# Kernel tuning notes

Measured on AMD Instinct MI355X. Metric: run time of the kernel, lower is better.

## Reference

```python
import jax, jax.numpy as jnp
import numpy as np

B, T, D, H, DH, DMLP, L, V = 32, 80, 128, 8, 64, 512, 8, 50257


def _ln(x, g, b, eps=1e-5):
    m = jnp.mean(x, axis=-1, keepdims=True)
    v = jnp.var(x, axis=-1, keepdims=True)
    return (x - m) * jax.lax.rsqrt(v + eps) * g + b


def setup_inputs() -> dict:
    key = jax.random.key(0)
    ks = jax.random.split(key, 16)
    emb_std = 1.0 / np.sqrt(2 * D)
    sD = 1.0 / np.sqrt(D)
    return {
        "x": jax.random.randint(ks[0], (B, T), 0, V),
        "tok_emb": jax.random.normal(ks[1], (V, D), jnp.float32) * emb_std,
        "pos_emb": jax.random.normal(ks[2], (T, D), jnp.float32) * emb_std,
        # per-block, per-head Q/K/V projections (no bias), stacked over L blocks
        "Wq": jax.random.normal(ks[3], (L, H, D, DH), jnp.float32) * sD,
        "Wk": jax.random.normal(ks[4], (L, H, D, DH), jnp.float32) * sD,
        "Wv": jax.random.normal(ks[5], (L, H, D, DH), jnp.float32) * sD,
        "Wo": jax.random.normal(ks[6], (L, H * DH, D), jnp.float32) / np.sqrt(H * DH),
        "bo": jnp.zeros((L, D), jnp.float32),
        "ln1_g": jnp.ones((L, D), jnp.float32),
        "ln1_b": jnp.zeros((L, D), jnp.float32),
        "ln2_g": jnp.ones((L, D), jnp.float32),
        "ln2_b": jnp.zeros((L, D), jnp.float32),
        "W1": jax.random.normal(ks[7], (L, D, DMLP), jnp.float32) * sD,
        "b1": jnp.zeros((L, DMLP), jnp.float32),
        "W2": jax.random.normal(ks[8], (L, DMLP, D), jnp.float32) / np.sqrt(DMLP),
        "b2": jnp.zeros((L, D), jnp.float32),
        "lnf_g": jnp.ones((D,), jnp.float32),
        "lnf_b": jnp.zeros((D,), jnp.float32),
        "Wcls": jax.random.normal(ks[9], (D, V), jnp.float32) * sD,
        "bcls": jnp.zeros((V,), jnp.float32),
    }


def reference(x, tok_emb, pos_emb, Wq, Wk, Wv, Wo, bo, ln1_g, ln1_b,
              ln2_g, ln2_b, W1, b1, W2, b2, lnf_g, lnf_b, Wcls, bcls):
    h = tok_emb[x] + pos_emb[jnp.arange(T)]  # [B,T,D]
    scale = 1.0 / np.sqrt(DH)

    def block(h, p):
        wq, wk, wv, wo, bo_, g1, b1_, g2, b2_, w1, bm1, w2, bm2 = p
        a = _ln(h, g1, b1_)
        q = jnp.einsum('btd,hde->bhte', a, wq)
        k = jnp.einsum('btd,hde->bhte', a, wk)
        v = jnp.einsum('btd,hde->bhte', a, wv)
        scores = jnp.einsum('bhte,bhse->bhts', q, k) * scale  # [B,H,T,T]
        # faithful to masked_fill(tril(scores)==0, -inf)
        scores = jnp.where(jnp.tril(scores) == 0, -jnp.inf, scores)
        w = jax.nn.softmax(scores, axis=-1)  # dropout inactive (eval)
        o = jnp.einsum('bhts,bhse->bhte', w, v)
        o = o.transpose(0, 2, 1, 3).reshape(h.shape[0], T, H * DH)
        h = h + o @ wo + bo_
        m = _ln(h, g2, b2_)
        h = h + jax.nn.gelu(m @ w1 + bm1, approximate=False) @ w2 + bm2
        return h, None

    h, _ = jax.lax.scan(
        block, h,
        (Wq, Wk, Wv, Wo, bo, ln1_g, ln1_b, ln2_g, ln2_b, W1, b1, W2, b2))
    h = _ln(h, lnf_g, lnf_b)
    return h @ Wcls + bcls  # [B,T,V]
```

## Files before the change

kernel.cpp:

```cpp
#include <hip/hip_runtime.h>
#include <hip/hip_bf16.h>
#include <hip/hip_fp16.h>
#include <math.h>

constexpr int B = 32, T = 80, D = 128, H = 8, DH = 64, DMLP = 512, L = 8, V = 50257;
constexpr int M = B * T;
constexpr int HD = H * DH;
constexpr int QKVN = 3 * HD;
constexpr int VPAD = 50304;

typedef _Float16 f16x8 __attribute__((ext_vector_type(8)));
typedef float f32x4 __attribute__((ext_vector_type(4)));

__device__ __forceinline__ float gelu_f(float x) {
    return 0.5f * x * (1.0f + erff(x * 0.70710678118654752f));
}

__global__ __launch_bounds__(256)
void embed_ln(const int* __restrict__ x, const float* __restrict__ tok,
              const float* __restrict__ pos, const float* __restrict__ g,
              const float* __restrict__ bb, float* __restrict__ h,
              __half* __restrict__ out) {
    int wid = threadIdx.x >> 6, lane = threadIdx.x & 63;
    int row = blockIdx.x * 4 + wid;
    int t = row % T;
    const float* te = tok + (size_t)x[row] * D;
    const float* pe = pos + (size_t)t * D;
    float v0 = te[lane]      + pe[lane];
    float v1 = te[64 + lane] + pe[64 + lane];
    int i0 = row * D + lane, i1 = i0 + 64;
    h[i0] = v0; h[i1] = v1;
    float s = v0 + v1;
    #pragma unroll
    for (int off = 32; off; off >>= 1) s += __shfl_xor(s, off);
    float mean = s * (1.0f / 128.0f);
    float d0 = v0 - mean, d1 = v1 - mean;
    float q = d0 * d0 + d1 * d1;
    #pragma unroll
    for (int off = 32; off; off >>= 1) q += __shfl_xor(q, off);
    float inv = rsqrtf(q * (1.0f / 128.0f) + 1e-5f);
    out[i0] = __float2half(d0 * inv * g[lane]      + bb[lane]);
    out[i1] = __float2half(d1 * inv * g[64 + lane] + bb[64 + lane]);
}

__global__ __launch_bounds__(256)
void combine_ln(const float* __restrict__ p, const float* __restrict__ bias,
                const float* __restrict__ g, const float* __restrict__ bb,
                float* __restrict__ h, __half* __restrict__ out) {
    constexpr int plane = M * D;
    int wid = threadIdx.x >> 6, lane = threadIdx.x & 63;
    int row = blockIdx.x * 4 + wid;
    int i0 = row * D + lane, i1 = i0 + 64;
    float v0 = h[i0] + p[i0] + p[i0 + plane] + p[i0 + 2 * plane] + p[i0 + 3 * plane]
             + bias[lane];
    float v1 = h[i1] + p[i1] + p[i1 + plane] + p[i1 + 2 * plane] + p[i1 + 3 * plane]
             + bias[64 + lane];
    h[i0] = v0; h[i1] = v1;
    float s = v0 + v1;
    #pragma unroll
    for (int off = 32; off; off >>= 1) s += __shfl_xor(s, off);
    float mean = s * (1.0f / 128.0f);
    float d0 = v0 - mean, d1 = v1 - mean;
    float q = d0 * d0 + d1 * d1;
    #pragma unroll
    for (int off = 32; off; off >>= 1) q += __shfl_xor(q, off);
    float inv = rsqrtf(q * (1.0f / 128.0f) + 1e-5f);
    out[i0] = __float2half(d0 * inv * g[lane]      + bb[lane]);
    out[i1] = __float2half(d1 * inv * g[64 + lane] + bb[64 + lane]);
}

__global__ __launch_bounds__(256)
void prep_small(const float* __restrict__ Wq, const float* __restrict__ Wk,
                const float* __restrict__ Wv, const float* __restrict__ Wo,
                const float* __restrict__ W1, const float* __restrict__ W2,
                __half* __restrict__ WqkvT, __half* __restrict__ WoT,
                __half* __restrict__ W1T, __half* __restrict__ W2T) {
    int id = blockIdx.x * 256 + threadIdx.x;
    if (id < L * QKVN * D) {
        int d = id & 127; int lc = id >> 7; int c = lc % QKVN; int l = lc / QKVN;
        int e = c & 63, hh = (c >> 6) & 7, wsel = c >> 9;
        const float* src = (wsel == 0) ? Wq : (wsel == 1) ? Wk : Wv;
        WqkvT[id] = __float2half(src[(((size_t)l * H + hh) * D + d) * DH + e]);
    } else {
        int id2 = id - L * QKVN * D;
        int which = id2 >> 19;
        int r = id2 & 524287;
        if (which == 0) {
            int k = r & 511, n = (r >> 9) & 127, l = r >> 16;
            WoT[r] = __float2half(Wo[((size_t)l * 512 + k) * 128 + n]);
        } else if (which == 1) {
            int k = r & 127, n = (r >> 7) & 511, l = r >> 16;
            W1T[r] = __float2half(W1[((size_t)l * 128 + k) * 512 + n]);
        } else {
            int k = r & 511, n = (r >> 9) & 127, l = r >> 16;
            W2T[r] = __float2half(W2[((size_t)l * 512 + k) * 128 + n]);
        }
    }
}

__global__ __launch_bounds__(256)
void prep_wcls(const float* __restrict__ Wcls, __half* __restrict__ WT) {
    __shared__ float tile[128][33];
    int n0 = blockIdx.x * 32;
    for (int i = threadIdx.x; i < 128 * 32; i += 256) {
        int k = i >> 5, j = i & 31;
        int n = n0 + j;
        tile[k][j] = (n < V) ? Wcls[(size_t)k * V + n] : 0.0f;
    }
    __syncthreads();
    for (int i = threadIdx.x; i < 32 * 64; i += 256) {
        int j = i >> 6, kp = i & 63;
        __half2 hv = __floats2half2_rn(tile[2 * kp][j], tile[2 * kp + 1][j]);
        *reinterpret_cast<__half2*>(WT + (size_t)(n0 + j) * 128 + 2 * kp) = hv;
    }
}

template<int MT, int NT, int MODE>
__global__ __launch_bounds__(256)
void hgemm(const __half* __restrict__ A, int lda,
           const __half* __restrict__ BT, int ldb,
           const float* __restrict__ bias,
           float* __restrict__ outF, __half* __restrict__ outH, int ldc) {
    const int tid = threadIdx.x, l = tid & 63, wid = tid >> 6;
    const int wm = wid >> 1, wn = wid & 1;
    const int row0 = blockIdx.y * (2 * MT * 16) + wm * (MT * 16);
    const int col0 = blockIdx.x * (2 * NT * 16) + wn * (NT * 16);
    const int z = blockIdx.z;
    const int rl = l & 15, kl = (l >> 4) * 8;
    const __half* Ap = A + (size_t)(row0 + rl) * lda + z * 128 + kl;
    const __half* Bp = BT + (size_t)(col0 + rl) * ldb + z * 128 + kl;

    f32x4 acc[MT][NT];
    #pragma unroll
    for (int mi = 0; mi < MT; mi++)
        #pragma unroll
        for (int ni = 0; ni < NT; ni++) acc[mi][ni] = (f32x4){0.f, 0.f, 0.f, 0.f};

    #pragma unroll
    for (int ks = 0; ks < 4; ks++) {
        f16x8 af[MT], bf[NT];
        #pragma unroll
        for (int mi = 0; mi < MT; mi++)
            af[mi] = *reinterpret_cast<const f16x8*>(Ap + (size_t)mi * 16 * lda + ks * 32);
        #pragma unroll
        for (int ni = 0; ni < NT; ni++)
            bf[ni] = *reinterpret_cast<const f16x8*>(Bp + (size_t)ni * 16 * ldb + ks * 32);
        #pragma unroll
        for (int mi = 0; mi < MT; mi++)
            #pragma unroll
            for (int ni = 0; ni < NT; ni++)
                acc[mi][ni] = __builtin_amdgcn_mfma_f32_16x16x32_f16(
                    af[mi], bf[ni], acc[mi][ni], 0, 0, 0);
    }

    const int orow = (l >> 4) * 4;
    #pragma unroll
    for (int mi = 0; mi < MT; mi++) {
        #pragma unroll
        for (int ni = 0; ni < NT; ni++) {
            int col = col0 + ni * 16 + rl;
            #pragma unroll
            for (int i = 0; i < 4; i++) {
                int row = row0 + mi * 16 + orow + i;
                float v = acc[mi][ni][i];
                if (MODE == 1) {
                    outF[((size_t)z * M + row) * 128 + col] = v;
                } else if (MODE == 2) {
                    outH[(size_t)row * ldc + col] = __float2half(gelu_f(v + bias[col]));
                } else {
                    outH[(size_t)row * ldc + col] = __float2half(v);
                }
            }
        }
    }
}

__global__ __launch_bounds__(256)
void hgemm_cls(const __half* __restrict__ A, const __half* __restrict__ BT,
               const float* __restrict__ bias, float* __restrict__ out) {
    constexpr int MT = 4, NT = 4;
    constexpr int MB = M / 128;
    constexpr int NB = VPAD / 128;
    constexpr int NWG = MB * NB;
    constexpr int q = NWG / 8, r = NWG % 8;
    int orig = blockIdx.x;
    int xcd = orig & 7, off = orig >> 3;
    int wg = (xcd < r ? xcd * (q + 1) : r * (q + 1) + (xcd - r) * q) + off;
    int mb = wg % MB, nb = wg / MB;

    const int tid = threadIdx.x, l = tid & 63, wid = tid >> 6;
    const int wm = wid >> 1, wn = wid & 1;
    const int row0 = mb * 128 + wm * 64;
    const int col0 = nb * 128 + wn * 64;
    const int rl = l & 15, kl = (l >> 4) * 8;
    const __half* Ap = A + (size_t)(row0 + rl) * 128 + kl;
    const __half* Bp = BT + (size_t)(col0 + rl) * 128 + kl;

    f32x4 acc[MT][NT];
    #pragma unroll
    for (int mi = 0; mi < MT; mi++)
        #pragma unroll
        for (int ni = 0; ni < NT; ni++) acc[mi][ni] = (f32x4){0.f, 0.f, 0.f, 0.f};

    #pragma unroll
    for (int ks = 0; ks < 4; ks++) {
        f16x8 af[MT], bf[NT];
        #pragma unroll
        for (int mi = 0; mi < MT; mi++)
            af[mi] = *reinterpret_cast<const f16x8*>(Ap + (size_t)mi * 16 * 128 + ks * 32);
        #pragma unroll
        for (int ni = 0; ni < NT; ni++)
            bf[ni] = *reinterpret_cast<const f16x8*>(Bp + (size_t)ni * 16 * 128 + ks * 32);
        #pragma unroll
        for (int mi = 0; mi < MT; mi++)
            #pragma unroll
            for (int ni = 0; ni < NT; ni++)
                acc[mi][ni] = __builtin_amdgcn_mfma_f32_16x16x32_f16(
                    af[mi], bf[ni], acc[mi][ni], 0, 0, 0);
    }

    const int orow = (l >> 4) * 4;
    #pragma unroll
    for (int mi = 0; mi < MT; mi++) {
        #pragma unroll
        for (int ni = 0; ni < NT; ni++) {
            int col = col0 + ni * 16 + rl;
            if (col < V) {
                float bv = bias[col];
                #pragma unroll
                for (int i = 0; i < 4; i++) {
                    int row = row0 + mi * 16 + orow + i;
                    out[(size_t)row * V + col] = acc[mi][ni][i] + bv;
                }
            }
        }
    }
}

__device__ __forceinline__ void load_h8(const __half* p, float* dst) {
    float4 raw = *reinterpret_cast<const float4*>(p);
    const __half2* h2 = reinterpret_cast<const __half2*>(&raw);
    float2 f;
    f = __half22float2(h2[0]); dst[0] = f.x; dst[1] = f.y;
    f = __half22float2(h2[1]); dst[2] = f.x; dst[3] = f.y;
    f = __half22float2(h2[2]); dst[4] = f.x; dst[5] = f.y;
    f = __half22float2(h2[3]); dst[6] = f.x; dst[7] = f.y;
}

__global__ __launch_bounds__(256)
void attn_fused(const __half* __restrict__ qkv, __half* __restrict__ o) {
    __shared__ float qS[T][DH];
    __shared__ float pS[T][T];
    int bh = blockIdx.x;
    int b = bh >> 3, h = bh & 7;
    const __half* base  = qkv + (size_t)b * T * QKVN + h * DH;
    const __half* kbase = base + HD;
    const __half* vbase = base + 2 * HD;

    for (int i = threadIdx.x; i < T * 8; i += 256) {
        int t = i >> 3, c8 = i & 7;
        load_h8(base + (size_t)t * QKVN + c8 * 8, &qS[t][c8 * 8]);
    }
    __syncthreads();

    for (int i = threadIdx.x; i < T * T; i += 256) {
        int t = i / T, s = i - t * T;
        float val = -INFINITY;
        if (s <= t) {
            const __half* krow = kbase + (size_t)s * QKVN;
            float accv = 0.0f;
            #pragma unroll
            for (int e8 = 0; e8 < 8; e8++) {
                float kf[8]; load_h8(krow + e8 * 8, kf);
                const float* qf = &qS[t][e8 * 8];
                #pragma unroll
                for (int u = 0; u < 8; u++) accv = fmaf(kf[u], qf[u], accv);
            }
            val = accv * 0.125f;
        }
        pS[t][s] = val;
    }
    __syncthreads();

    for (int i = threadIdx.x; i < T * 8; i += 256) {
        int t = i >> 3, c8 = i & 7;
        load_h8(vbase + (size_t)t * QKVN + c8 * 8, &qS[t][c8 * 8]);
    }

    int wid = threadIdx.x >> 6, lane = threadIdx.x & 63;
    for (int t = wid; t < T; t += 4) {
        float v0 = pS[t][lane];
        float v1 = (lane < T - 64) ? pS[t][64 + lane] : -INFINITY;
        float mx = fmaxf(v0, v1);
        #pragma unroll
        for (int off = 32; off; off >>= 1) mx = fmaxf(mx, __shfl_xor(mx, off));
        float e0 = expf(v0 - mx);
        float e1 = (lane < T - 64) ? expf(v1 - mx) : 0.0f;
        float ss = e0 + e1;
        #pragma unroll
        for (int off = 32; off; off >>= 1) ss += __shfl_xor(ss, off);
        float rs = 1.0f / ss;
        pS[t][lane] = e0 * rs;
        if (lane < T - 64) pS[t][64 + lane] = e1 * rs;
    }
    __syncthreads();

    for (int i = threadIdx.x; i < T * DH; i += 256) {
        int t = i >> 6, e = i & 63;
        float accv = 0.0f;
        for (int s = 0; s <= t; s++) accv = fmaf(pS[t][s], qS[s][e], accv);
        o[((size_t)b * T + t) * HD + h * DH + e] = __float2half(accv);
    }
}

extern "C" void kernel_launch(void* const* d_in, const int* in_sizes, int n_in,
                              void* d_out, int out_size, void* d_ws, size_t ws_size,
                              hipStream_t stream) {
    const int*   x     = (const int*)d_in[0];
    const float* tok   = (const float*)d_in[1];
    const float* pos   = (const float*)d_in[2];
    const float* Wq    = (const float*)d_in[3];
    const float* Wk    = (const float*)d_in[4];
    const float* Wv    = (const float*)d_in[5];
    const float* Wo    = (const float*)d_in[6];
    const float* bo    = (const float*)d_in[7];
    const float* ln1g  = (const float*)d_in[8];
    const float* ln1b  = (const float*)d_in[9];
    const float* ln2g  = (const float*)d_in[10];
    const float* ln2b  = (const float*)d_in[11];
    const float* W1    = (const float*)d_in[12];
    const float* b1    = (const float*)d_in[13];
    const float* W2    = (const float*)d_in[14];
    const float* b2    = (const float*)d_in[15];
    const float* lnfg  = (const float*)d_in[16];
    const float* lnfb  = (const float*)d_in[17];
    const float* Wcls  = (const float*)d_in[18];
    const float* bcls  = (const float*)d_in[19];
    float* out = (float*)d_out;

    char* w = (char*)d_ws;
    float*  h     = (float*)w;                 w += (size_t)M * D * 4;
    __half* a_h   = (__half*)w;                w += (size_t)M * D * 2;
    __half* qkvh  = (__half*)w;                w += (size_t)M * QKVN * 2;
    __half* o_h   = (__half*)w;                w += (size_t)M * HD * 2;
    __half* mlp   = (__half*)w;                w += (size_t)M * DMLP * 2;
    float*  pbuf  = (float*)w;                 w += (size_t)4 * M * D * 4;
    __half* WqkvT = (__half*)w;                w += (size_t)L * QKVN * D * 2;
    __half* WoT   = (__half*)w;                w += (size_t)L * D * HD * 2;
    __half* W1T   = (__half*)w;                w += (size_t)L * DMLP * D * 2;
    __half* W2T   = (__half*)w;                w += (size_t)L * D * DMLP * 2;
    __half* WclsT = (__half*)w;                w += (size_t)VPAD * D * 2;

    prep_small<<<(L * QKVN * D + 3 * L * DMLP * D) / 256, 256, 0, stream>>>(
        Wq, Wk, Wv, Wo, W1, W2, WqkvT, WoT, W1T, W2T);
    prep_wcls<<<VPAD / 32, 256, 0, stream>>>(Wcls, WclsT);
    embed_ln<<<M / 4, 256, 0, stream>>>(x, tok, pos, ln1g, ln1b, h, a_h);

    for (int l = 0; l < L; l++) {
        hgemm<2, 2, 3><<<dim3(QKVN / 64, M / 64, 1), 256, 0, stream>>>(
            a_h, D, WqkvT + (size_t)l * QKVN * D, D, nullptr, nullptr, qkvh, QKVN);
        attn_fused<<<B * H, 256, 0, stream>>>(qkvh, o_h);
        hgemm<2, 2, 1><<<dim3(D / 64, M / 64, 4), 256, 0, stream>>>(
            o_h, HD, WoT + (size_t)l * D * HD, HD, nullptr, pbuf, nullptr, D);
        combine_ln<<<M / 4, 256, 0, stream>>>(
            pbuf, bo + l * D, ln2g + l * D, ln2b + l * D, h, a_h);

        hgemm<2, 2, 2><<<dim3(DMLP / 64, M / 64, 1), 256, 0, stream>>>(
            a_h, D, W1T + (size_t)l * DMLP * D, D, b1 + l * DMLP, nullptr, mlp, DMLP);
        hgemm<2, 2, 1><<<dim3(D / 64, M / 64, 4), 256, 0, stream>>>(
            mlp, DMLP, W2T + (size_t)l * D * DMLP, DMLP, nullptr, pbuf, nullptr, D);
        const float* ng = (l + 1 < L) ? ln1g + (l + 1) * D : lnfg;
        const float* nb = (l + 1 < L) ? ln1b + (l + 1) * D : lnfb;
        combine_ln<<<M / 4, 256, 0, stream>>>(pbuf, b2 + l * D, ng, nb, h, a_h);
    }

    hgemm_cls<<<(M / 128) * (VPAD / 128), 256, 0, stream>>>(a_h, WclsT, bcls, out);
}
```

Before: 1.427 ms.

## Fuse QKV projection into MFMA-based attention and deepen split-K for projections

Removes the separate QKV GEMM and its global intermediate. Each attention block now computes its head's Q, K and V directly from the normalized activations with MFMA, keeping them in LDS. The QK^T and PV products move from scalar fp32 loops to f16 MFMA tiles: probabilities are stored as f16 and V is kept transposed with zero padding. The Wo and W2 GEMMs switch from 4 to 8 split-K partitions for more parallelism, so the combine kernel must read twice as many partial planes. The trade-off is a lower-precision P·V path and recomputed weight loads in every attention block.

```diff
diff --git a/kernel.cpp b/kernel.cpp
--- a/kernel.cpp
+++ b/kernel.cpp
@@ -51,10 +51,10 @@
     int wid = threadIdx.x >> 6, lane = threadIdx.x & 63;
     int row = blockIdx.x * 4 + wid;
     int i0 = row * D + lane, i1 = i0 + 64;
-    float v0 = h[i0] + p[i0] + p[i0 + plane] + p[i0 + 2 * plane] + p[i0 + 3 * plane]
-             + bias[lane];
-    float v1 = h[i1] + p[i1] + p[i1 + plane] + p[i1 + 2 * plane] + p[i1 + 3 * plane]
-             + bias[64 + lane];
+    float v0 = h[i0] + bias[lane];
+    float v1 = h[i1] + bias[64 + lane];
+    #pragma unroll
+    for (int k = 0; k < 8; k++) { v0 += p[i0 + k * plane]; v1 += p[i1 + k * plane]; }
     h[i0] = v0; h[i1] = v1;
     float s = v0 + v1;
     #pragma unroll
@@ -115,7 +115,7 @@
     }
 }
 
-template<int MT, int NT, int MODE>
+template<int MT, int NT, int KS, int MODE>
 __global__ __launch_bounds__(256)
 void hgemm(const __half* __restrict__ A, int lda,
            const __half* __restrict__ BT, int ldb,
@@ -127,8 +127,8 @@
     const int col0 = blockIdx.x * (2 * NT * 16) + wn * (NT * 16);
     const int z = blockIdx.z;
     const int rl = l & 15, kl = (l >> 4) * 8;
-    const __half* Ap = A + (size_t)(row0 + rl) * lda + z * 128 + kl;
-    const __half* Bp = BT + (size_t)(col0 + rl) * ldb + z * 128 + kl;
+    const __half* Ap = A + (size_t)(row0 + rl) * lda + z * (KS * 32) + kl;
+    const __half* Bp = BT + (size_t)(col0 + rl) * ldb + z * (KS * 32) + kl;
 
     f32x4 acc[MT][NT];
     #pragma unroll
@@ -137,7 +137,7 @@
         for (int ni = 0; ni < NT; ni++) acc[mi][ni] = (f32x4){0.f, 0.f, 0.f, 0.f};
 
     #pragma unroll
-    for (int ks = 0; ks < 4; ks++) {
+    for (int ks = 0; ks < KS; ks++) {
         f16x8 af[MT], bf[NT];
         #pragma unroll
         for (int mi = 0; mi < MT; mi++)
@@ -165,10 +165,8 @@
                 float v = acc[mi][ni][i];
                 if (MODE == 1) {
                     outF[((size_t)z * M + row) * 128 + col] = v;
-                } else if (MODE == 2) {
+                } else {
                     outH[(size_t)row * ldc + col] = __float2half(gelu_f(v + bias[col]));
-                } else {
-                    outH[(size_t)row * ldc + col] = __float2half(v);
                 }
             }
         }
@@ -237,79 +235,106 @@
     }
 }
 
-__device__ __forceinline__ void load_h8(const __half* p, float* dst) {
-    float4 raw = *reinterpret_cast<const float4*>(p);
-    const __half2* h2 = reinterpret_cast<const __half2*>(&raw);
-    float2 f;
-    f = __half22float2(h2[0]); dst[0] = f.x; dst[1] = f.y;
-    f = __half22float2(h2[1]); dst[2] = f.x; dst[3] = f.y;
-    f = __half22float2(h2[2]); dst[4] = f.x; dst[5] = f.y;
-    f = __half22float2(h2[3]); dst[6] = f.x; dst[7] = f.y;
-}
-
-__global__ __launch_bounds__(256)
-void attn_fused(const __half* __restrict__ qkv, __half* __restrict__ o) {
-    __shared__ float qS[T][DH];
-    __shared__ float pS[T][T];
-    int bh = blockIdx.x;
-    int b = bh >> 3, h = bh & 7;
-    const __half* base  = qkv + (size_t)b * T * QKVN + h * DH;
-    const __half* kbase = base + HD;
-    const __half* vbase = base + 2 * HD;
-
-    for (int i = threadIdx.x; i < T * 8; i += 256) {
-        int t = i >> 3, c8 = i & 7;
-        load_h8(base + (size_t)t * QKVN + c8 * 8, &qS[t][c8 * 8]);
+__global__ __launch_bounds__(256)
+void attn_layer(const __half* __restrict__ a, const __half* __restrict__ Wl,
+                __half* __restrict__ o) {
+    __shared__ __align__(16) char smem[62208];
+    __half* qS = (__half*)smem;
+    __half* kS = (__half*)(smem + 11520);
+    __half* vT = (__half*)(smem + 23040);
+    __half* aS = (__half*)(smem + 35328);
+    float*  pS = (float*)(smem + 35328);
+    __half* pH = (__half*)smem;
+
+    const int bh = blockIdx.x, b = bh >> 3, hh = bh & 7;
+    const int tid = threadIdx.x, l = tid & 63, wid = tid >> 6;
+    const int rl = l & 15, kq = (l >> 4) * 8, orow = (l >> 4) * 4;
+
+    const __half* arow = a + (size_t)b * T * D;
+    for (int i = tid; i < T * 16; i += 256) {
+        int t = i >> 4, c = i & 15;
+        *reinterpret_cast<float4*>(aS + t * 136 + c * 8) =
+            *reinterpret_cast<const float4*>(arow + t * 128 + c * 8);
+    }
+    for (int i = tid; i < 64 * 16; i += 256) {
+        int e = i >> 4, j = i & 15;
+        vT[e * 96 + 80 + j] = __float2half(0.f);
     }
     __syncthreads();
 
-    for (int i = threadIdx.x; i < T * T; i += 256) {
-        int t = i / T, s = i - t * T;
-        float val = -INFINITY;
-        if (s <= t) {
-            const __half* krow = kbase + (size_t)s * QKVN;
-            float accv = 0.0f;
+    for (int tile = wid; tile < 60; tile += 4) {
+        int which = tile / 20, sub = tile % 20, mt = sub >> 2, nt = sub & 3;
+        int col = which * 512 + hh * 64 + nt * 16 + rl;
+        const __half* Bp  = Wl + (size_t)col * 128 + kq;
+        const __half* Apl = aS + (mt * 16 + rl) * 136 + kq;
+        f32x4 acc = (f32x4){0.f, 0.f, 0.f, 0.f};
+        #pragma unroll
+        for (int ks = 0; ks < 4; ks++)
+            acc = __builtin_amdgcn_mfma_f32_16x16x32_f16(
+                *reinterpret_cast<const f16x8*>(Apl + ks * 32),
+                *reinterpret_cast<const f16x8*>(Bp + ks * 32), acc, 0, 0, 0);
+        if (which == 2) {
             #pragma unroll
-            for (int e8 = 0; e8 < 8; e8++) {
-                float kf[8]; load_h8(krow + e8 * 8, kf);
-                const float* qf = &qS[t][e8 * 8];
-                #pragma unroll
-                for (int u = 0; u < 8; u++) accv = fmaf(kf[u], qf[u], accv);
-            }
-            val = accv * 0.125f;
+            for (int i = 0; i < 4; i++)
+                vT[(nt * 16 + rl) * 96 + mt * 16 + orow + i] = __float2half(acc[i]);
+        } else {
+            __half* dst = (which == 0) ? qS : kS;
+            #pragma unroll
+            for (int i = 0; i < 4; i++)
+                dst[(mt * 16 + orow + i) * 72 + nt * 16 + rl] = __float2half(acc[i]);
         }
-        pS[t][s] = val;
     }
     __syncthreads();
 
-    for (int i = threadIdx.x; i < T * 8; i += 256) {
-        int t = i >> 3, c8 = i & 7;
-        load_h8(vbase + (size_t)t * QKVN + c8 * 8, &qS[t][c8 * 8]);
-    }
-
-    int wid = threadIdx.x >> 6, lane = threadIdx.x & 63;
+    for (int tile = wid; tile < 25; tile += 4) {
+        int mt = tile / 5, st = tile % 5;
+        const __half* Aq = qS + (mt * 16 + rl) * 72 + kq;
+        const __half* Bk = kS + (st * 16 + rl) * 72 + kq;
+        f32x4 acc = (f32x4){0.f, 0.f, 0.f, 0.f};
+        #pragma unroll
+        for (int ks = 0; ks < 2; ks++)
+            acc = __builtin_amdgcn_mfma_f32_16x16x32_f16(
+                *reinterpret_cast<const f16x8*>(Aq + ks * 32),
+                *reinterpret_cast<const f16x8*>(Bk + ks * 32), acc, 0, 0, 0);
+        #pragma unroll
+        for (int i = 0; i < 4; i++) {
+            int t = mt * 16 + orow + i, s = st * 16 + rl;
+            pS[t * 84 + s] = (s <= t) ? acc[i] * 0.125f : -INFINITY;
+        }
+    }
+    __syncthreads();
+
     for (int t = wid; t < T; t += 4) {
-        float v0 = pS[t][lane];
-        float v1 = (lane < T - 64) ? pS[t][64 + lane] : -INFINITY;
+        float v0 = pS[t * 84 + l];
+        float v1 = (l < 16) ? pS[t * 84 + 64 + l] : -INFINITY;
         float mx = fmaxf(v0, v1);
         #pragma unroll
         for (int off = 32; off; off >>= 1) mx = fmaxf(mx, __shfl_xor(mx, off));
         float e0 = expf(v0 - mx);
-        float e1 = (lane < T - 64) ? expf(v1 - mx) : 0.0f;
+        float e1 = (l < 16) ? expf(v1 - mx) : 0.0f;
         float ss = e0 + e1;
         #pragma unroll
         for (int off = 32; off; off >>= 1) ss += __shfl_xor(ss, off);
         float rs = 1.0f / ss;
-        pS[t][lane] = e0 * rs;
-        if (lane < T - 64) pS[t][64 + lane] = e1 * rs;
+        pH[t * 96 + l] = __float2half(e0 * rs);
+        if (l < 32) pH[t * 96 + 64 + l] = __float2half((l < 16) ? e1 * rs : 0.0f);
     }
     __syncthreads();
 
-    for (int i = threadIdx.x; i < T * DH; i += 256) {
-        int t = i >> 6, e = i & 63;
-        float accv = 0.0f;
-        for (int s = 0; s <= t; s++) accv = fmaf(pS[t][s], qS[s][e], accv);
-        o[((size_t)b * T + t) * HD + h * DH + e] = __float2half(accv);
+    for (int tile = wid; tile < 20; tile += 4) {
+        int mt = tile >> 2, et = tile & 3;
+        const __half* Apv = pH + (mt * 16 + rl) * 96 + kq;
+        const __half* Bv  = vT + (et * 16 + rl) * 96 + kq;
+        f32x4 acc = (f32x4){0.f, 0.f, 0.f, 0.f};
+        #pragma unroll
+        for (int ks = 0; ks < 3; ks++)
+            acc = __builtin_amdgcn_mfma_f32_16x16x32_f16(
+                *reinterpret_cast<const f16x8*>(Apv + ks * 32),
+                *reinterpret_cast<const f16x8*>(Bv + ks * 32), acc, 0, 0, 0);
+        #pragma unroll
+        for (int i = 0; i < 4; i++)
+            o[((size_t)b * T + mt * 16 + orow + i) * HD + hh * 64 + et * 16 + rl]
+                = __float2half(acc[i]);
     }
 }
 
@@ -341,10 +366,9 @@
     char* w = (char*)d_ws;
     float*  h     = (float*)w;                 w += (size_t)M * D * 4;
     __half* a_h   = (__half*)w;                w += (size_t)M * D * 2;
-    __half* qkvh  = (__half*)w;                w += (size_t)M * QKVN * 2;
     __half* o_h   = (__half*)w;                w += (size_t)M * HD * 2;
     __half* mlp   = (__half*)w;                w += (size_t)M * DMLP * 2;
-    float*  pbuf  = (float*)w;                 w += (size_t)4 * M * D * 4;
+    float*  pbuf  = (float*)w;                 w += (size_t)8 * M * D * 4;
     __half* WqkvT = (__half*)w;                w += (size_t)L * QKVN * D * 2;
     __half* WoT   = (__half*)w;                w += (size_t)L * D * HD * 2;
     __half* W1T   = (__half*)w;                w += (size_t)L * DMLP * D * 2;
@@ -357,17 +381,16 @@
     embed_ln<<<M / 4, 256, 0, stream>>>(x, tok, pos, ln1g, ln1b, h, a_h);
 
     for (int l = 0; l < L; l++) {
-        hgemm<2, 2, 3><<<dim3(QKVN / 64, M / 64, 1), 256, 0, stream>>>(
-            a_h, D, WqkvT + (size_t)l * QKVN * D, D, nullptr, nullptr, qkvh, QKVN);
-        attn_fused<<<B * H, 256, 0, stream>>>(qkvh, o_h);
-        hgemm<2, 2, 1><<<dim3(D / 64, M / 64, 4), 256, 0, stream>>>(
+        attn_layer<<<B * H, 256, 0, stream>>>(
+            a_h, WqkvT + (size_t)l * QKVN * D, o_h);
+        hgemm<2, 2, 2, 1><<<dim3(D / 64, M / 64, 8), 256, 0, stream>>>(
             o_h, HD, WoT + (size_t)l * D * HD, HD, nullptr, pbuf, nullptr, D);
         combine_ln<<<M / 4, 256, 0, stream>>>(
             pbuf, bo + l * D, ln2g + l * D, ln2b + l * D, h, a_h);
 
-        hgemm<2, 2, 2><<<dim3(DMLP / 64, M / 64, 1), 256, 0, stream>>>(
+        hgemm<2, 2, 4, 2><<<dim3(DMLP / 64, M / 64, 1), 256, 0, stream>>>(
             a_h, D, W1T + (size_t)l * DMLP * D, D, b1 + l * DMLP, nullptr, mlp, DMLP);
-        hgemm<2, 2, 1><<<dim3(D / 64, M / 64, 4), 256, 0, stream>>>(
+        hgemm<2, 2, 2, 1><<<dim3(D / 64, M / 64, 8), 256, 0, stream>>>(
             mlp, DMLP, W2T + (size_t)l * D * DMLP, DMLP, nullptr, pbuf, nullptr, D);
         const float* ng = (l + 1 < L) ? ln1g + (l + 1) * D : lnfg;
         const float* nb = (l + 1 < L) ? ln1b + (l + 1) * D : lnfb;
```

Result: faster. 1.225 ms (-14.1%).
